# Optimization experiments

Hardware: AMD Instinct MI355X
Metric: run time of the kernel (lower is better)

## Reference

```python
import jax, jax.numpy as jnp
import numpy as np

B, N, F = 16, 4096, 3

def setup_inputs() -> dict:
    key = jax.random.key(0)
    k1, k2 = jax.random.split(key)
    array1 = jax.random.normal(k1, (B, N, F), dtype=jnp.float32)
    array2 = jax.random.normal(k2, (B, N, F), dtype=jnp.float32)
    return {"array1": array1, "array2": array2}

def reference(array1, array2):
    # D[b, i, j] = ||array1[b, i] - array2[b, j]||^2, via expansion identity
    sq1 = jnp.sum(array1 * array1, axis=-1)              # [B, N1]
    sq2 = jnp.sum(array2 * array2, axis=-1)              # [B, N2]
    cross = jnp.einsum('bnd,bmd->bnm', array1, array2)   # [B, N1, N2]
    D = sq1[:, :, None] + sq2[:, None, :] - 2.0 * cross  # [B, N1, N2]
    # av_dist1: for each sample in array2, min dist to array1, then mean
    av_dist1 = jnp.mean(jnp.min(D, axis=1), axis=1)      # [B]
    # av_dist2: for each sample in array1, min dist to array2, then mean
    av_dist2 = jnp.mean(jnp.min(D, axis=2), axis=1)      # [B]
    dist = jnp.mean(0.5 * av_dist1 + 0.5 * av_dist2)
    return dist * 100.0
```

## Files before the change

### kernel.cpp

```cpp
#include <hip/hip_runtime.h>


constexpr int B_ = 16;
constexpr int N_ = 4096;
constexpr int BN = B_ * N_;
constexpr int BLK = 256;
constexpr int JSPLIT = 2;
constexpr int JCHUNK = N_ / JSPLIT;
constexpr int JT2 = JCHUNK / 16;

using bf16x8 = __attribute__((ext_vector_type(8))) __bf16;
using f32x4  = __attribute__((ext_vector_type(4))) float;

__device__ inline uint bf16_rne(float f) {
    uint u = __float_as_uint(f);
    return (u + 0x7FFFu + ((u >> 16) & 1u)) >> 16;
}
__device__ inline float bf16_f(uint h) { return __uint_as_float(h << 16); }

__global__ __launch_bounds__(BLK)
void prep_kernel(const float* __restrict__ a1, const float* __restrict__ a2,
                 uint4* __restrict__ A1, uint4* __restrict__ B1,
                 uint4* __restrict__ A2, uint4* __restrict__ B2) {
    int gi = blockIdx.x * BLK + threadIdx.x;
    const float* in = blockIdx.y ? a2 : a1;
    uint4* Ao = blockIdx.y ? A2 : A1;
    uint4* Bo = blockIdx.y ? B2 : B1;
    float x = in[3 * gi], y = in[3 * gi + 1], z = in[3 * gi + 2];
    float sq = fmaf(x, x, fmaf(y, y, z * z));
    float t = -0.5f * sq;
    uint hx = bf16_rne(x), hy = bf16_rne(y), hz = bf16_rne(z);
    uint lx = bf16_rne(x - bf16_f(hx));
    uint ly = bf16_rne(y - bf16_f(hy));
    uint lz = bf16_rne(z - bf16_f(hz));
    uint th = bf16_rne(t);
    uint tl = bf16_rne(t - bf16_f(th));
    const uint ONE = 0x3F80u;
    Ao[2 * gi]     = make_uint4(hx | (hy << 16), hz | (lx << 16), ly | (lz << 16), hx | (hy << 16));
    Ao[2 * gi + 1] = make_uint4(hz | (ONE << 16), ONE | (th << 16), tl, 0u);
    Bo[2 * gi]     = make_uint4(hx | (hy << 16), hz | (hx << 16), hy | (hz << 16), lx | (ly << 16));
    Bo[2 * gi + 1] = make_uint4(lz | (th << 16), tl | (ONE << 16), ONE, 0u);
}

#define FOLD1(Q) {                                                               \
    f32x4 o0 = __builtin_amdgcn_mfma_f32_16x16x32_bf16(a0, (Q), cz, 0, 0, 0);    \
    f32x4 o1 = __builtin_amdgcn_mfma_f32_16x16x32_bf16(a1, (Q), cz, 0, 0, 0);    \
    f32x4 o2 = __builtin_amdgcn_mfma_f32_16x16x32_bf16(a2, (Q), cz, 0, 0, 0);    \
    f32x4 o3 = __builtin_amdgcn_mfma_f32_16x16x32_bf16(a3, (Q), cz, 0, 0, 0);    \
    _Pragma("unroll")                                                            \
    for (int r = 0; r < 4; ++r) {                                                \
        vm0[r] = fmaxf(fmaxf(vm0[r], o0[r]), o1[r]);                             \
        vm1[r] = fmaxf(fmaxf(vm1[r], o2[r]), o3[r]);                             \
    } }
#undef FOLD1

#define FOLDT(Q) {                                                               \
    f32x4 o0 = __builtin_amdgcn_mfma_f32_16x16x32_bf16(a0, (Q), cz, 0, 0, 0);    \
    f32x4 o1 = __builtin_amdgcn_mfma_f32_16x16x32_bf16(a1, (Q), cz, 0, 0, 0);    \
    f32x4 o2 = __builtin_amdgcn_mfma_f32_16x16x32_bf16(a2, (Q), cz, 0, 0, 0);    \
    f32x4 o3 = __builtin_amdgcn_mfma_f32_16x16x32_bf16(a3, (Q), cz, 0, 0, 0);    \
    _Pragma("unroll")                                                            \
    for (int r = 0; r < 4; ++r) {                                                \
        vm0[r] = fmaxf(vm0[r], o0[r]);                                           \
        vm1[r] = fmaxf(vm1[r], o1[r]);                                           \
        vm2[r] = fmaxf(vm2[r], o2[r]);                                           \
        vm3[r] = fmaxf(vm3[r], o3[r]);                                           \
    } }

__global__ __launch_bounds__(BLK, 4)
void minmax_kernel(const uint4* __restrict__ A1u, const uint4* __restrict__ B1u,
                   const uint4* __restrict__ A2u, const uint4* __restrict__ B2u,
                   float* __restrict__ vout) {
    int z = blockIdx.z, b = blockIdx.y;
    int d = z >> 1, s = z & 1;
    const bf16x8* __restrict__ Aarr = (const bf16x8*)(d ? A2u : A1u);
    const bf16x8* __restrict__ Barr = (const bf16x8*)(d ? B1u : B2u);
    int tid = threadIdx.x;
    int L = tid & 63, w = tid >> 6;
    int lpt = L & 15, hi = (L >> 4) & 1;
    bool act = L < 32;
    int ibase = blockIdx.x * 256 + w * 64;

    const bf16x8* pA = Aarr + (size_t)(b * N_ + ibase + lpt) * 2 + hi;
    const bf16x8* pB = Barr + (size_t)(b * N_ + s * JCHUNK + lpt) * 2 + hi;

    uint4 zu; zu.x = zu.y = zu.z = zu.w = 0u;
    bf16x8 zf = __builtin_bit_cast(bf16x8, zu);
    bf16x8 a0 = act ? pA[0] : zf;
    bf16x8 a1 = act ? pA[32] : zf;
    bf16x8 a2 = act ? pA[64] : zf;
    bf16x8 a3 = act ? pA[96] : zf;
    f32x4 cz = {0.f, 0.f, 0.f, 0.f};
    f32x4 vm0 = {-3.0e38f, -3.0e38f, -3.0e38f, -3.0e38f};
    f32x4 vm1 = vm0, vm2 = vm0, vm3 = vm0;

    bf16x8 p0 = pB[0], p1 = pB[32], p2 = pB[64], p3 = pB[96];
#pragma unroll 1
    for (int jt = 0; jt < JT2 - 4; jt += 4) {
        bf16x8 n0 = pB[(size_t)(jt + 4) * 32], n1 = pB[(size_t)(jt + 5) * 32];
        bf16x8 n2 = pB[(size_t)(jt + 6) * 32], n3 = pB[(size_t)(jt + 7) * 32];
        FOLDT(p0) FOLDT(p1) FOLDT(p2) FOLDT(p3)
        p0 = n0; p1 = n1; p2 = n2; p3 = n3;
    }
    FOLDT(p0) FOLDT(p1) FOLDT(p2) FOLDT(p3)

#pragma unroll
    for (int off = 1; off < 16; off <<= 1)
#pragma unroll
        for (int r = 0; r < 4; ++r) {
            vm0[r] = fmaxf(vm0[r], __shfl_xor(vm0[r], off));
            vm1[r] = fmaxf(vm1[r], __shfl_xor(vm1[r], off));
            vm2[r] = fmaxf(vm2[r], __shfl_xor(vm2[r], off));
            vm3[r] = fmaxf(vm3[r], __shfl_xor(vm3[r], off));
        }
    if (lpt == 0) {
        int rg = L >> 4;
#pragma unroll
        for (int r = 0; r < 4; ++r) {
            int row = rg * 4 + r;
            int o = z * BN + b * N_ + ibase + row;
            vout[o] = vm0[r];
            vout[o + 16] = vm1[r];
            vout[o + 32] = vm2[r];
            vout[o + 48] = vm3[r];
        }
    }
}

__device__ inline float block_sum_256(float v, float* red4) {
    for (int off = 32; off; off >>= 1) v += __shfl_down(v, off, 64);
    int lane = threadIdx.x & 63, w = threadIdx.x >> 6;
    if (lane == 0) red4[w] = v;
    __syncthreads();
    return red4[0] + red4[1] + red4[2] + red4[3];
}

__global__ __launch_bounds__(BLK)
void reduce1_kernel(const float* __restrict__ vout, float* __restrict__ sums) {
    int t = blockIdx.x * BLK + threadIdx.x;
    float m0 = fmaxf(vout[t], vout[BN + t]);
    float m1 = fmaxf(vout[2 * BN + t], vout[3 * BN + t]);
    float v = -2.0f * (m0 + m1);
    __shared__ float red4[4];
    float sm = block_sum_256(v, red4);
    if (threadIdx.x == 0) sums[blockIdx.x] = sm;
}

__global__ __launch_bounds__(BLK)
void reduce2_kernel(const float* __restrict__ sums, float* __restrict__ out) {
    float v = sums[threadIdx.x];
    __shared__ float red4[4];
    float sm = block_sum_256(v, red4);
    if (threadIdx.x == 0) out[0] = sm * (50.0f / (float)BN);
}

extern "C" void kernel_launch(void* const* d_in, const int* in_sizes, int n_in,
                              void* d_out, int out_size, void* d_ws, size_t ws_size,
                              hipStream_t stream) {
    const float* a1 = (const float*)d_in[0];
    const float* a2 = (const float*)d_in[1];
    char* ws = (char*)d_ws;
    uint4* A1 = (uint4*)(ws);
    uint4* B1 = (uint4*)(ws + (2u << 20));
    uint4* A2 = (uint4*)(ws + (4u << 20));
    uint4* B2 = (uint4*)(ws + (6u << 20));
    float* vout = (float*)(ws + (8u << 20));
    float* sums = (float*)(ws + (9u << 20));
    float* out = (float*)d_out;

    prep_kernel<<<dim3(BN / BLK, 2), BLK, 0, stream>>>(a1, a2, A1, B1, A2, B2);
    minmax_kernel<<<dim3(N_ / 256, B_, 2 * JSPLIT), BLK, 0, stream>>>(A1, B1, A2, B2, vout);
    reduce1_kernel<<<dim3(BN / BLK), BLK, 0, stream>>>(vout, sums);
    reduce2_kernel<<<dim3(1), BLK, 0, stream>>>(sums, out);
}
```

Before: 41.67 us.

## Stage B tiles in LDS per block and fold two tiles per iteration

Each block now cooperatively loads its whole 2048-point B chunk (64 KB) into shared memory once, then all four waves read B fragments from LDS instead of each wave streaming them from global memory. The inner loop processes two B tiles per iteration with eight independent MFMAs, merging pairs of results with nested fmax. Launch bounds are lowered to 2 blocks per CU, presumably because the 64 KB LDS footprint limits occupancy anyway. The trade-off is lower occupancy and an upfront load-then-sync phase with no overlap, in exchange for less redundant global and L2 traffic.

```diff
diff --git a/kernel.cpp b/kernel.cpp
--- a/kernel.cpp
+++ b/kernel.cpp
@@ -42,48 +42,47 @@
     Bo[2 * gi + 1] = make_uint4(lz | (th << 16), tl | (ONE << 16), ONE, 0u);
 }
 
-#define FOLD1(Q) {                                                               \
-    f32x4 o0 = __builtin_amdgcn_mfma_f32_16x16x32_bf16(a0, (Q), cz, 0, 0, 0);    \
-    f32x4 o1 = __builtin_amdgcn_mfma_f32_16x16x32_bf16(a1, (Q), cz, 0, 0, 0);    \
-    f32x4 o2 = __builtin_amdgcn_mfma_f32_16x16x32_bf16(a2, (Q), cz, 0, 0, 0);    \
-    f32x4 o3 = __builtin_amdgcn_mfma_f32_16x16x32_bf16(a3, (Q), cz, 0, 0, 0);    \
+#define FOLDP(Qa, Qb) {                                                          \
+    f32x4 oA = __builtin_amdgcn_mfma_f32_16x16x32_bf16(a0, (Qa), cz, 0, 0, 0);   \
+    f32x4 oB = __builtin_amdgcn_mfma_f32_16x16x32_bf16(a1, (Qa), cz, 0, 0, 0);   \
+    f32x4 oC = __builtin_amdgcn_mfma_f32_16x16x32_bf16(a2, (Qa), cz, 0, 0, 0);   \
+    f32x4 oD = __builtin_amdgcn_mfma_f32_16x16x32_bf16(a3, (Qa), cz, 0, 0, 0);   \
+    f32x4 oE = __builtin_amdgcn_mfma_f32_16x16x32_bf16(a0, (Qb), cz, 0, 0, 0);   \
+    f32x4 oF = __builtin_amdgcn_mfma_f32_16x16x32_bf16(a1, (Qb), cz, 0, 0, 0);   \
+    f32x4 oG = __builtin_amdgcn_mfma_f32_16x16x32_bf16(a2, (Qb), cz, 0, 0, 0);   \
+    f32x4 oH = __builtin_amdgcn_mfma_f32_16x16x32_bf16(a3, (Qb), cz, 0, 0, 0);   \
     _Pragma("unroll")                                                            \
     for (int r = 0; r < 4; ++r) {                                                \
-        vm0[r] = fmaxf(fmaxf(vm0[r], o0[r]), o1[r]);                             \
-        vm1[r] = fmaxf(fmaxf(vm1[r], o2[r]), o3[r]);                             \
-    } }
-#undef FOLD1
-
-#define FOLDT(Q) {                                                               \
-    f32x4 o0 = __builtin_amdgcn_mfma_f32_16x16x32_bf16(a0, (Q), cz, 0, 0, 0);    \
-    f32x4 o1 = __builtin_amdgcn_mfma_f32_16x16x32_bf16(a1, (Q), cz, 0, 0, 0);    \
-    f32x4 o2 = __builtin_amdgcn_mfma_f32_16x16x32_bf16(a2, (Q), cz, 0, 0, 0);    \
-    f32x4 o3 = __builtin_amdgcn_mfma_f32_16x16x32_bf16(a3, (Q), cz, 0, 0, 0);    \
-    _Pragma("unroll")                                                            \
-    for (int r = 0; r < 4; ++r) {                                                \
-        vm0[r] = fmaxf(vm0[r], o0[r]);                                           \
-        vm1[r] = fmaxf(vm1[r], o1[r]);                                           \
-        vm2[r] = fmaxf(vm2[r], o2[r]);                                           \
-        vm3[r] = fmaxf(vm3[r], o3[r]);                                           \
+        vm0[r] = fmaxf(fmaxf(vm0[r], oA[r]), oE[r]);                             \
+        vm1[r] = fmaxf(fmaxf(vm1[r], oB[r]), oF[r]);                             \
+        vm2[r] = fmaxf(fmaxf(vm2[r], oC[r]), oG[r]);                             \
+        vm3[r] = fmaxf(fmaxf(vm3[r], oD[r]), oH[r]);                             \
     } }
 
-__global__ __launch_bounds__(BLK, 4)
+__global__ __launch_bounds__(BLK, 2)
 void minmax_kernel(const uint4* __restrict__ A1u, const uint4* __restrict__ B1u,
                    const uint4* __restrict__ A2u, const uint4* __restrict__ B2u,
                    float* __restrict__ vout) {
+    __shared__ uint4 smem[JT2 * 32];
     int z = blockIdx.z, b = blockIdx.y;
     int d = z >> 1, s = z & 1;
     const bf16x8* __restrict__ Aarr = (const bf16x8*)(d ? A2u : A1u);
-    const bf16x8* __restrict__ Barr = (const bf16x8*)(d ? B1u : B2u);
+    const uint4*  __restrict__ Bu   = (d ? B1u : B2u);
     int tid = threadIdx.x;
     int L = tid & 63, w = tid >> 6;
-    int lpt = L & 15, hi = (L >> 4) & 1;
+    int lpt = L & 15;
     bool act = L < 32;
     int ibase = blockIdx.x * 256 + w * 64;
+    int j0 = s * JCHUNK;
 
-    const bf16x8* pA = Aarr + (size_t)(b * N_ + ibase + lpt) * 2 + hi;
-    const bf16x8* pB = Barr + (size_t)(b * N_ + s * JCHUNK + lpt) * 2 + hi;
+#pragma unroll
+    for (int k = 0; k < 16; ++k) {
+        int F = k * 256 + tid;
+        int t = F >> 5, sl = F & 31;
+        smem[F] = Bu[(size_t)(b * N_ + j0 + (t << 4) + (sl & 15)) * 2 + (sl >> 4)];
+    }
 
+    const bf16x8* pA = Aarr + (size_t)(b * N_ + ibase + lpt) * 2 + ((L >> 4) & 1);
     uint4 zu; zu.x = zu.y = zu.z = zu.w = 0u;
     bf16x8 zf = __builtin_bit_cast(bf16x8, zu);
     bf16x8 a0 = act ? pA[0] : zf;
@@ -94,15 +93,15 @@
     f32x4 vm0 = {-3.0e38f, -3.0e38f, -3.0e38f, -3.0e38f};
     f32x4 vm1 = vm0, vm2 = vm0, vm3 = vm0;
 
-    bf16x8 p0 = pB[0], p1 = pB[32], p2 = pB[64], p3 = pB[96];
-#pragma unroll 1
-    for (int jt = 0; jt < JT2 - 4; jt += 4) {
-        bf16x8 n0 = pB[(size_t)(jt + 4) * 32], n1 = pB[(size_t)(jt + 5) * 32];
-        bf16x8 n2 = pB[(size_t)(jt + 6) * 32], n3 = pB[(size_t)(jt + 7) * 32];
-        FOLDT(p0) FOLDT(p1) FOLDT(p2) FOLDT(p3)
-        p0 = n0; p1 = n1; p2 = n2; p3 = n3;
+    __syncthreads();
+
+    int lslot = L & 31;
+#pragma unroll 2
+    for (int t = 0; t < JT2; t += 2) {
+        bf16x8 q0 = __builtin_bit_cast(bf16x8, smem[t * 32 + lslot]);
+        bf16x8 q1 = __builtin_bit_cast(bf16x8, smem[t * 32 + 32 + lslot]);
+        FOLDP(q0, q1)
     }
-    FOLDT(p0) FOLDT(p1) FOLDT(p2) FOLDT(p3)
 
 #pragma unroll
     for (int off = 1; off < 16; off <<= 1)
```

After: 42.59 us. 1.02x slower.
